# Optimization experiments

Measured on AMD Instinct MI355X. Metric: run time of the kernel, lower is better.

## Reference

```python
import jax, jax.numpy as jnp
import numpy as np

H = 768; B = 8; T = 1024; V = 50257
S = 256      # token_distribution_samples
K = 64       # token_topk
POOL = 1024  # max(S*4, K) token pool
TEMP = 0.1; LIM = 0.25; MW = 0.1


def _ln(x, g, b):
    m = x.mean(-1, keepdims=True)
    v = ((x - m) ** 2).mean(-1, keepdims=True)
    return (x - m) / jnp.sqrt(v + 1e-5) * g + b


def _head(x, g, b, w1, b1, w2, b2):
    # LayerNorm -> Linear -> GELU(exact) -> (Dropout=identity in eval) -> Linear
    h = _ln(x, g, b) @ w1 + b1
    h = jax.nn.gelu(h, approximate=False)
    return h @ w2 + b2


def _l2norm(x):
    return x / jnp.maximum(jnp.linalg.norm(x, axis=-1, keepdims=True), 1e-12)


def setup_inputs() -> dict:
    key = jax.random.key(0)
    ks = jax.random.split(key, 16)
    init = lambda k, shp: jax.random.normal(k, shp, jnp.float32) * 0.02
    f32 = jnp.float32
    return {
        "latent": jax.random.normal(ks[0], (B, T, H), f32),
        "token_embedding_matrix": jax.random.normal(ks[1], (V, H), f32),
        # scale head
        "scale_ln_g": jnp.ones((H,), f32), "scale_ln_b": jnp.zeros((H,), f32),
        "scale_w1": init(ks[2], (H, H)), "scale_b1": jnp.zeros((H,), f32),
        "scale_w2": init(ks[3], (H, H)), "scale_b2": jnp.zeros((H,), f32),
        # bias head
        "bias_ln_g": jnp.ones((H,), f32), "bias_ln_b": jnp.zeros((H,), f32),
        "bias_w1": init(ks[4], (H, H)), "bias_b1": jnp.zeros((H,), f32),
        "bias_w2": init(ks[5], (H, H)), "bias_b2": jnp.zeros((H,), f32),
        # contrastive head (projection_dim == H)
        "con_ln_g": jnp.ones((H,), f32), "con_ln_b": jnp.zeros((H,), f32),
        "con_w1": init(ks[6], (H, H)), "con_b1": jnp.zeros((H,), f32),
        "con_w2": init(ks[7], (H, H)), "con_b2": jnp.zeros((H,), f32),
        # deterministic augmentation noise (randn_like * 0.01)
        "noise_a": jax.random.normal(ks[8], (B * T, H), f32) * 0.01,
        "noise_b": jax.random.normal(ks[9], (B * T, H), f32) * 0.01,
        # deterministic row-sampling (torch.randperm analogues)
        "samp_idx": jax.random.permutation(ks[10], B * T)[:S].astype(jnp.int32),
        "tok_idx": jax.random.permutation(ks[11], V)[:POOL].astype(jnp.int32),
    }


def reference(latent, token_embedding_matrix,
              scale_ln_g, scale_ln_b, scale_w1, scale_b1, scale_w2, scale_b2,
              bias_ln_g, bias_ln_b, bias_w1, bias_b1, bias_w2, bias_b2,
              con_ln_g, con_ln_b, con_w1, con_b1, con_w2, con_b2,
              noise_a, noise_b, samp_idx, tok_idx):
    # compensate: u = s(z)*z + b(z)
    scale = 1.0 + LIM * jnp.tanh(_head(latent, scale_ln_g, scale_ln_b, scale_w1, scale_b1, scale_w2, scale_b2))
    bias = LIM * jnp.tanh(_head(latent, bias_ln_g, bias_ln_b, bias_w1, bias_b1, bias_w2, bias_b2))
    aligned = scale * latent + bias

    flat = aligned.reshape(-1, H)  # [N, H], N = B*T
    # contrastive loss
    va = _l2norm(_head(flat + noise_a, con_ln_g, con_ln_b, con_w1, con_b1, con_w2, con_b2))
    vb = _l2norm(_head(flat + noise_b, con_ln_g, con_ln_b, con_w1, con_b1, con_w2, con_b2))
    logits = va @ vb.T / TEMP  # [N, N]
    loss_ab = -jnp.mean(jnp.diagonal(jax.nn.log_softmax(logits, axis=-1)))
    loss_ba = -jnp.mean(jnp.diagonal(jax.nn.log_softmax(logits.T, axis=-1)))
    con_loss = 0.5 * (loss_ab + loss_ba)

    # token distribution loss
    af = flat[samp_idx]                     # [S, H]
    te = token_embedding_matrix[tok_idx]    # [POOL, H]
    tl = _l2norm(af) @ _l2norm(te).T / TEMP  # [S, POOL]
    top_vals, top_idx = jax.lax.top_k(tl, K)
    top_emb = te[top_idx]                   # [S, K, H] gather
    w = jax.nn.softmax(top_vals, axis=-1)[..., None]
    proto = (w * top_emb).sum(axis=1)       # [S, H]
    proto_loss = jnp.mean((af - proto) ** 2)
    moment_loss = jnp.mean((af.mean(0) - te.mean(0)) ** 2) \
        + jnp.mean((af.std(0) - te.std(0)) ** 2)
    token_dist_loss = proto_loss + MW * moment_loss

    comp_reg_loss = jnp.mean((scale - 1.0) ** 2) + jnp.mean(bias ** 2)
    return (aligned, con_loss, token_dist_loss, comp_reg_loss, scale, bias)
```

## Files before the change

### kernel.cpp

```cpp
#include <hip/hip_runtime.h>
#include <hip/hip_bf16.h>

typedef __hip_bfloat16 bf16;
typedef __attribute__((ext_vector_type(4))) float f32x4;
typedef __attribute__((ext_vector_type(8))) short bf16x8v;

static constexpr int   HD    = 768;
static constexpr int   NRr   = 8192;
static constexpr int   SSAMP = 256;
static constexpr int   KTOP  = 64;
static constexpr int   NPOOL = 1024;
static constexpr float TINV  = 10.0f;

__device__ __forceinline__ float bf2f(bf16 h){ return __bfloat162float(h); }
__device__ __forceinline__ bf16  f2bf(float f){ return __float2bfloat16(f); }

__device__ __forceinline__ float gelu_exact(float x){
  return 0.5f * x * (1.0f + erff(x * 0.70710678118654752f));
}

__device__ __forceinline__ float block_sum(float v, float* buf){
  const int lane = threadIdx.x & 63, w = threadIdx.x >> 6;
  const int nw = (int)blockDim.x >> 6;
  #pragma unroll
  for(int o = 32; o; o >>= 1) v += __shfl_down(v, o);
  __syncthreads();
  if(lane == 0) buf[w] = v;
  __syncthreads();
  float t = 0.f;
  for(int i = 0; i < nw; i++) t += buf[i];
  return t;
}

__device__ __forceinline__ void block_sum2(float& a, float& b, float* buf){
  const int lane = threadIdx.x & 63, w = threadIdx.x >> 6;
  #pragma unroll
  for(int o = 32; o; o >>= 1){ a += __shfl_down(a, o); b += __shfl_down(b, o); }
  __syncthreads();
  if(lane == 0){ buf[w] = a; buf[4 + w] = b; }
  __syncthreads();
  float ta = 0.f, tb = 0.f;
  #pragma unroll
  for(int i = 0; i < 4; i++){ ta += buf[i]; tb += buf[4 + i]; }
  a = ta; b = tb;
}

__device__ __forceinline__ void gload_lds16(const bf16* g, bf16* lds_uniform){
  __builtin_amdgcn_global_load_lds(
      (const __attribute__((address_space(1))) unsigned int*)(const void*)g,
      (__attribute__((address_space(3))) unsigned int*)(void*)lds_uniform,
      16, 0, 0);
}

struct TsA { const float* w[6]; const float* gg[6]; bf16* o[6]; };
__global__ __launch_bounds__(256)
void tscale6(TsA a){
  __shared__ float t[32][33];
  const int z = blockIdx.z;
  const float* Win = a.w[z];
  const float* g   = a.gg[z];
  bf16* Wt         = a.o[z];
  const int tx = threadIdx.x, ty = threadIdx.y;
  const int bx = blockIdx.x * 32, by = blockIdx.y * 32;
  #pragma unroll
  for(int j = 0; j < 4; j++)
    t[ty + j*8][tx] = Win[(size_t)(by + ty + j*8) * HD + bx + tx];
  __syncthreads();
  const float gv = g ? g[by + tx] : 1.0f;
  #pragma unroll
  for(int j = 0; j < 4; j++)
    Wt[(size_t)(bx + ty + j*8) * HD + by + tx] = f2bf(gv * t[tx][ty + j*8]);
}

struct FbA { const float* bln[3]; const float* w1[3]; const float* b1[3]; float* o[3]; };
__global__ __launch_bounds__(256)
void foldbias3(FbA a){
  __shared__ float red[4][64];
  const int h = blockIdx.y;
  const int lane = threadIdx.x & 63, w = threadIdx.x >> 6;
  const int n = blockIdx.x * 64 + lane;
  const float* bl = a.bln[h];
  const float* w1 = a.w1[h];
  float t = 0.f;
  for(int k = w * 192; k < w * 192 + 192; k++)
    t += bl[k] * w1[(size_t)k * HD + n];
  red[w][lane] = t;
  __syncthreads();
  if(w == 0)
    a.o[h][n] = a.b1[h][n] + red[0][lane] + red[1][lane] + red[2][lane] + red[3][lane];
}

__global__ __launch_bounds__(256)
void lnxh_kernel(const float* __restrict__ x, bf16* __restrict__ o){
  __shared__ float buf[4];
  const int row = blockIdx.x, tid = threadIdx.x;
  const size_t base = (size_t)row * HD;
  float v[3];
  #pragma unroll
  for(int j = 0; j < 3; j++) v[j] = x[base + tid + j*256];
  float s = v[0] + v[1] + v[2];
  s = block_sum(s, buf);
  const float m = s * (1.0f / HD);
  float q = 0.f;
  #pragma unroll
  for(int j = 0; j < 3; j++){ const float d = v[j] - m; q += d*d; }
  q = block_sum(q, buf);
  const float inv = rsqrtf(q * (1.0f / HD) + 1e-5f);
  #pragma unroll
  for(int j = 0; j < 3; j++)
    o[base + tid + j*256] = f2bf((v[j] - m) * inv);
}

__global__ __launch_bounds__(256)
void fuse_al_ln(const float* __restrict__ latent, const float* __restrict__ sc,
                const float* __restrict__ bi, const float* __restrict__ na,
                const float* __restrict__ nb, float* __restrict__ out_aligned,
                bf16* __restrict__ X){
  __shared__ float buf[8];
  const int row = blockIdx.x, tid = threadIdx.x;
  const size_t base = (size_t)row * HD;
  float ua[3], ub[3];
  #pragma unroll
  for(int j = 0; j < 3; j++){
    const int i = tid + j*256;
    const float a = sc[base + i] * latent[base + i] + bi[base + i];
    out_aligned[base + i] = a;
    ua[j] = a + na[base + i];
    ub[j] = a + nb[base + i];
  }
  float sa = ua[0] + ua[1] + ua[2];
  float sb = ub[0] + ub[1] + ub[2];
  block_sum2(sa, sb, buf);
  const float ma = sa * (1.0f / HD), mb = sb * (1.0f / HD);
  float qa = 0.f, qb = 0.f;
  #pragma unroll
  for(int j = 0; j < 3; j++){
    const float da = ua[j] - ma; qa += da*da;
    const float db = ub[j] - mb; qb += db*db;
  }
  block_sum2(qa, qb, buf);
  const float ia = rsqrtf(qa * (1.0f / HD) + 1e-5f);
  const float ib = rsqrtf(qb * (1.0f / HD) + 1e-5f);
  #pragma unroll
  for(int j = 0; j < 3; j++){
    const int i = tid + j*256;
    X[base + i] = f2bf((ua[j] - ma) * ia);
    X[(size_t)(row + NRr) * HD + i] = f2bf((ub[j] - mb) * ib);
  }
}

enum { EPI_GELU = 0, EPI_SB = 1, EPI_RAW = 3, EPI_LOGITS = 4, EPI_TL = 5 };

template<int EPI>
__global__ __launch_bounds__(256, 2)
void gemm_kernel(const bf16* __restrict__ A, const bf16* __restrict__ Bt,
                 const bf16* __restrict__ Bt2,
                 const int M, const int N, const int K,
                 const int lda, const int ldc,
                 const float* __restrict__ bias, const float* __restrict__ bias2,
                 bf16* __restrict__ outb, float* __restrict__ outf,
                 float* __restrict__ outf2,
                 float* __restrict__ aux, float* __restrict__ aux2){
  __shared__ __align__(16) bf16 As[128 * 64];
  __shared__ __align__(16) bf16 Bs[128 * 64];
  __shared__ float rbuf[512];

  const int tid  = threadIdx.x;
  const int wave = tid >> 6, lane = tid & 63;
  const int wm = wave >> 1, wn = wave & 1;
  const int r16 = lane & 15, kh = lane >> 4;
  const int bx = blockIdx.x, by = blockIdx.y;
  const int row0 = by * 128, col0 = bx * 128;

  float addv = 0.f;
  if constexpr(EPI == EPI_SB){
    if(blockIdx.z == 0){ addv = 1.0f; }
    else { A += 768; Bt = Bt2; bias = bias2; outf = outf2; }
  }

  f32x4 acc[4][4];
  #pragma unroll
  for(int i = 0; i < 4; i++)
    #pragma unroll
    for(int j = 0; j < 4; j++){ f32x4 z = {0.f,0.f,0.f,0.f}; acc[i][j] = z; }

  const bf16* gA[4]; const bf16* gB[4];
  bf16* lA[4]; bf16* lB[4];
  #pragma unroll
  for(int j = 0; j < 4; j++){
    const int c = tid + j*256;
    const int rr = c >> 3, p = c & 7;
    const int g = (p - (rr & 7)) & 7;
    gA[j] = A  + (size_t)(row0 + rr) * lda + g * 8;
    gB[j] = Bt + (size_t)(col0 + rr) * K   + g * 8;
    lA[j] = As + ((size_t)j*256 + wave*64) * 8;
    lB[j] = Bs + ((size_t)j*256 + wave*64) * 8;
  }
  const int sw = r16 & 7;

  for(int k0 = 0; k0 < K; k0 += 64){
    __syncthreads();
    #pragma unroll
    for(int j = 0; j < 4; j++){
      gload_lds16(gA[j] + k0, lA[j]);
      gload_lds16(gB[j] + k0, lB[j]);
    }
    __syncthreads();
    #pragma unroll
    for(int kk = 0; kk < 2; kk++){
      const int koff = ((kk*4 + kh + sw) & 7) * 8;
      bf16x8v av[4], bv[4];
      #pragma unroll
      for(int f = 0; f < 4; f++){
        av[f] = *(const bf16x8v*)(As + (wm*64 + f*16 + r16) * 64 + koff);
        bv[f] = *(const bf16x8v*)(Bs + (wn*64 + f*16 + r16) * 64 + koff);
      }
      #pragma unroll
      for(int i = 0; i < 4; i++)
        #pragma unroll
        for(int j = 0; j < 4; j++)
          acc[i][j] = __builtin_amdgcn_mfma_f32_16x16x32_bf16(av[i], bv[j], acc[i][j], 0, 0, 0);
    }
  }

  const int crow0 = row0 + wm * 64;
  const int ccol0 = col0 + wn * 64;

  if constexpr(EPI != EPI_LOGITS){
    float part = 0.f;
    #pragma unroll
    for(int i = 0; i < 4; i++){
      #pragma unroll
      for(int j = 0; j < 4; j++){
        const int col = ccol0 + j*16 + r16;
        const float bvv = bias ? bias[col] : 0.f;
        #pragma unroll
        for(int q = 0; q < 4; q++){
          const int row = crow0 + i*16 + kh*4 + q;
          const float v = acc[i][j][q] + bvv;
          const size_t off = (size_t)row * ldc + col;
          if constexpr(EPI == EPI_GELU){
            outb[off] = f2bf(gelu_exact(v));
          } else if constexpr(EPI == EPI_SB){
            const float t = 0.25f * tanhf(v);
            outf[off] = t + addv;
            part += t * t;
          } else if constexpr(EPI == EPI_TL){
            outf[off] = v * TINV;
          } else {
            outb[off] = f2bf(v);
          }
        }
      }
    }
    if constexpr(EPI == EPI_SB){
      const float tot2 = block_sum(part, rbuf);
      if(tid == 0)
        aux[(size_t)blockIdx.z * (gridDim.x * gridDim.y) + by * gridDim.x + bx] = tot2;
    }
  } else {
    float rs[16], cs[4];
    #pragma unroll
    for(int t = 0; t < 16; t++) rs[t] = 0.f;
    #pragma unroll
    for(int t = 0; t < 4; t++) cs[t] = 0.f;
    #pragma unroll
    for(int i = 0; i < 4; i++)
      #pragma unroll
      for(int j = 0; j < 4; j++)
        #pragma unroll
        for(int q = 0; q < 4; q++){
          const float ev = expf(acc[i][j][q] * TINV);
          rs[i*4 + q] += ev;
          cs[j]       += ev;
        }
    #pragma unroll
    for(int t = 0; t < 16; t++){
      float r = rs[t];
      r += __shfl_xor(r, 1); r += __shfl_xor(r, 2);
      r += __shfl_xor(r, 4); r += __shfl_xor(r, 8);
      rs[t] = r;
    }
    if(r16 == 0){
      #pragma unroll
      for(int i = 0; i < 4; i++)
        #pragma unroll
        for(int q = 0; q < 4; q++)
          rbuf[wn*128 + wm*64 + i*16 + kh*4 + q] = rs[i*4 + q];
    }
    #pragma unroll
    for(int j = 0; j < 4; j++){
      float c = cs[j];
      c += __shfl_xor(c, 16); c += __shfl_xor(c, 32);
      cs[j] = c;
    }
    if(kh == 0){
      #pragma unroll
      for(int j = 0; j < 4; j++)
        rbuf[256 + wm*128 + wn*64 + j*16 + r16] = cs[j];
    }
    __syncthreads();
    if(tid < 128){
      aux [(size_t)bx * M + row0 + tid] = rbuf[tid]       + rbuf[128 + tid];
      aux2[(size_t)by * M + col0 + tid] = rbuf[256 + tid] + rbuf[384 + tid];
    }
  }
}

__global__ __launch_bounds__(256)
void l2n_kernel(bf16* __restrict__ vio){
  __shared__ float buf[4];
  const int row = blockIdx.x, tid = threadIdx.x;
  const size_t base = (size_t)row * HD;
  float v[3];
  #pragma unroll
  for(int j = 0; j < 3; j++) v[j] = bf2f(vio[base + tid + j*256]);
  float q = v[0]*v[0] + v[1]*v[1] + v[2]*v[2];
  q = block_sum(q, buf);
  const float inv = 1.0f / fmaxf(sqrtf(q), 1e-12f);
  #pragma unroll
  for(int j = 0; j < 3; j++) vio[base + tid + j*256] = f2bf(v[j] * inv);
}

__global__ __launch_bounds__(256)
void diag_kernel(const bf16* __restrict__ va, const bf16* __restrict__ vb,
                 float* __restrict__ diag){
  const int lane = threadIdx.x & 63;
  const int row = blockIdx.x * 4 + (threadIdx.x >> 6);
  const size_t base = (size_t)row * HD;
  float d = 0.f;
  #pragma unroll
  for(int j = 0; j < 12; j++){
    const int i = lane + j*64;
    d += bf2f(va[base + i]) * bf2f(vb[base + i]);
  }
  #pragma unroll
  for(int o = 32; o; o >>= 1) d += __shfl_down(d, o);
  if(lane == 0) diag[row] = d * TINV;
}

__global__ __launch_bounds__(256)
void rcsum_kernel(const float* __restrict__ rp, const float* __restrict__ cp,
                  float* __restrict__ rs, float* __restrict__ cs, const int nb){
  const int i = blockIdx.x * 256 + threadIdx.x;
  float r = 0.f, c = 0.f;
  for(int b = 0; b < nb; b++){
    r += rp[(size_t)b * NRr + i];
    c += cp[(size_t)b * NRr + i];
  }
  rs[i] = r; cs[i] = c;
}

__global__ __launch_bounds__(256)
void af_kernel(const float* __restrict__ aligned, const int* __restrict__ samp,
               float* __restrict__ afraw, bf16* __restrict__ afn){
  __shared__ float buf[4];
  const int s = blockIdx.x, tid = threadIdx.x;
  const size_t src = (size_t)samp[s] * HD, dst = (size_t)s * HD;
  float v[3];
  #pragma unroll
  for(int j = 0; j < 3; j++){
    const int i = tid + j*256;
    v[j] = aligned[src + i];
    afraw[dst + i] = v[j];
  }
  float q = v[0]*v[0] + v[1]*v[1] + v[2]*v[2];
  q = block_sum(q, buf);
  const float inv = 1.0f / fmaxf(sqrtf(q), 1e-12f);
  #pragma unroll
  for(int j = 0; j < 3; j++) afn[dst + tid + j*256] = f2bf(v[j] * inv);
}

__global__ __launch_bounds__(256)
void te_kernel(const float* __restrict__ emb, const int* __restrict__ tok,
               float* __restrict__ teg, bf16* __restrict__ ten){
  __shared__ float buf[4];
  const int p = blockIdx.x, tid = threadIdx.x;
  const size_t src = (size_t)tok[p] * HD, dst = (size_t)p * HD;
  float v[3];
  #pragma unroll
  for(int j = 0; j < 3; j++){
    const int i = tid + j*256;
    v[j] = emb[src + i];
    teg[dst + i] = v[j];
  }
  float q = v[0]*v[0] + v[1]*v[1] + v[2]*v[2];
  q = block_sum(q, buf);
  const float inv = 1.0f / fmaxf(sqrtf(q), 1e-12f);
  #pragma unroll
  for(int j = 0; j < 3; j++) ten[dst + tid + j*256] = f2bf(v[j] * inv);
}

__global__ __launch_bounds__(256)
void topk_kernel(const float* __restrict__ tl, const float* __restrict__ teg,
                 const float* __restrict__ afraw, float* __restrict__ protopart){
  __shared__ float sv[NPOOL];
  __shared__ float topv[KTOP];
  __shared__ int   topi[KTOP];
  __shared__ float wts[KTOP];
  __shared__ float rv[4];
  __shared__ int   ri[4];
  __shared__ float buf[4];
  __shared__ float sinv;
  const int s = blockIdx.x, tid = threadIdx.x;
  const int lane = tid & 63, w = tid >> 6;
  #pragma unroll
  for(int j = 0; j < 4; j++) sv[tid + j*256] = tl[(size_t)s * NPOOL + tid + j*256];
  __syncthreads();
  for(int k = 0; k < KTOP; k++){
    float bvv = -1e30f; int bi = 0x7fffffff;
    #pragma unroll
    for(int j = 0; j < 4; j++){
      const int i = tid + j*256;
      const float x = sv[i];
      if(x > bvv || (x == bvv && i < bi)){ bvv = x; bi = i; }
    }
    #pragma unroll
    for(int o = 1; o < 64; o <<= 1){
      const float ov = __shfl_xor(bvv, o);
      const int   oi = __shfl_xor(bi, o);
      if(ov > bvv || (ov == bvv && oi < bi)){ bvv = ov; bi = oi; }
    }
    if(lane == 0){ rv[w] = bvv; ri[w] = bi; }
    __syncthreads();
    if(tid == 0){
      for(int w2 = 1; w2 < 4; w2++)
        if(rv[w2] > bvv || (rv[w2] == bvv && ri[w2] < bi)){ bvv = rv[w2]; bi = ri[w2]; }
      if(bi < 0 || bi >= NPOOL) bi = 0;
      topv[k] = bvv; topi[k] = bi; sv[bi] = -1e30f;
    }
    __syncthreads();
  }
  if(tid < KTOP) wts[tid] = expf(topv[tid] - topv[0]);
  __syncthreads();
  if(tid == 0){
    float t = 0.f;
    for(int k = 0; k < KTOP; k++) t += wts[k];
    sinv = 1.0f / t;
  }
  __syncthreads();
  float part = 0.f;
  #pragma unroll
  for(int j = 0; j < 3; j++){
    const int h = tid + j*256;
    float ph = 0.f;
    for(int k = 0; k < KTOP; k++) ph += wts[k] * teg[(size_t)topi[k] * HD + h];
    ph *= sinv;
    const float d = afraw[(size_t)s * HD + h] - ph;
    part += d * d;
  }
  part = block_sum(part, buf);
  if(tid == 0) protopart[s] = part;
}

__global__ __launch_bounds__(768)
void mom1_kernel(const float* __restrict__ afraw, const float* __restrict__ teg,
                 float* __restrict__ partial){
  const int b = blockIdx.x, h = threadIdx.x;
  float sa = 0.f, sa2 = 0.f, st = 0.f, st2 = 0.f;
  for(int r = b * 40; r < b * 40 + 40; r++){
    if(r < SSAMP){
      const float v = afraw[(size_t)r * HD + h];
      sa += v; sa2 += v * v;
    } else {
      const float v = teg[(size_t)(r - SSAMP) * HD + h];
      st += v; st2 += v * v;
    }
  }
  partial[(size_t)(b*4 + 0) * HD + h] = sa;
  partial[(size_t)(b*4 + 1) * HD + h] = sa2;
  partial[(size_t)(b*4 + 2) * HD + h] = st;
  partial[(size_t)(b*4 + 3) * HD + h] = st2;
}

__global__ __launch_bounds__(768)
void mom2_kernel(const float* __restrict__ partial, float* __restrict__ mom){
  __shared__ float buf[12];
  const int h = threadIdx.x;
  float sa = 0.f, sa2 = 0.f, st = 0.f, st2 = 0.f;
  for(int b = 0; b < 32; b++){
    sa  += partial[(size_t)(b*4 + 0) * HD + h];
    sa2 += partial[(size_t)(b*4 + 1) * HD + h];
    st  += partial[(size_t)(b*4 + 2) * HD + h];
    st2 += partial[(size_t)(b*4 + 3) * HD + h];
  }
  const float ma  = sa * (1.0f / SSAMP);
  const float sda = sqrtf(fmaxf(sa2 * (1.0f / SSAMP) - ma * ma, 0.f));
  const float mt  = st * (1.0f / NPOOL);
  const float sdt = sqrtf(fmaxf(st2 * (1.0f / NPOOL) - mt * mt, 0.f));
  const float dmu = ma - mt, dsd = sda - sdt;
  const float t1 = block_sum(dmu * dmu, buf);
  const float t2 = block_sum(dsd * dsd, buf);
  if(h == 0){ mom[0] = t1; mom[1] = t2; }
}

__global__ __launch_bounds__(1024)
void final_kernel(const float* __restrict__ rs, const float* __restrict__ cs,
                  const float* __restrict__ diag,
                  const float* __restrict__ aux, const int naux,
                  const float* __restrict__ protopart, const float* __restrict__ mom,
                  float* __restrict__ outsc){
  __shared__ float buf[16];
  const int tid = threadIdx.x;
  float s1 = 0.f, s2 = 0.f;
  for(int r = tid; r < NRr; r += 1024){
    const float dg = diag[r];
    s1 += logf(rs[r]) - dg;
    s2 += logf(cs[r]) - dg;
  }
  float c1 = 0.f;
  for(int j = tid; j < naux; j += 1024) c1 += aux[j];
  float pp = 0.f;
  for(int j = tid; j < SSAMP; j += 1024) pp += protopart[j];
  s1 = block_sum(s1, buf);
  s2 = block_sum(s2, buf);
  c1 = block_sum(c1, buf);
  pp = block_sum(pp, buf);
  if(tid == 0){
    const float con  = 0.5f * (s1 + s2) / (float)NRr;
    const float creg = c1 / 6291456.0f;
    const float tdl  = pp / (float)(SSAMP * HD) + 0.1f * ((mom[0] + mom[1]) / (float)HD);
    outsc[0] = con;
    outsc[1] = tdl;
    outsc[2] = creg;
  }
}

extern "C" void kernel_launch(void* const* d_in, const int* in_sizes, int n_in,
                              void* d_out, int out_size, void* d_ws, size_t ws_size,
                              hipStream_t stream){
  (void)in_sizes; (void)n_in; (void)out_size; (void)ws_size;
  const float* latent = (const float*)d_in[0];
  const float* tokemb = (const float*)d_in[1];
  const float* s_g  = (const float*)d_in[2];  const float* s_bln = (const float*)d_in[3];
  const float* s_w1 = (const float*)d_in[4];  const float* s_b1  = (const float*)d_in[5];
  const float* s_w2 = (const float*)d_in[6];  const float* s_b2  = (const float*)d_in[7];
  const float* b_g  = (const float*)d_in[8];  const float* b_bln = (const float*)d_in[9];
  const float* b_w1 = (const float*)d_in[10]; const float* b_b1  = (const float*)d_in[11];
  const float* b_w2 = (const float*)d_in[12]; const float* b_b2  = (const float*)d_in[13];
  const float* c_g  = (const float*)d_in[14]; const float* c_bln = (const float*)d_in[15];
  const float* c_w1 = (const float*)d_in[16]; const float* c_b1  = (const float*)d_in[17];
  const float* c_w2 = (const float*)d_in[18]; const float* c_b2  = (const float*)d_in[19];
  const float* noise_a = (const float*)d_in[20];
  const float* noise_b = (const float*)d_in[21];
  const int*  samp = (const int*)d_in[22];
  const int*  tok  = (const int*)d_in[23];

  float* out = (float*)d_out;
  float* out_aligned = out;
  float* out_scalars = out + (size_t)NRr * HD;
  float* out_scale   = out + (size_t)NRr * HD + 3;
  float* out_bias    = out_scale + (size_t)NRr * HD;

  char* wp = (char*)d_ws;
  auto alloc = [&](size_t bytes) -> char* {
    char* p = wp; wp += (bytes + 255) & ~(size_t)255; return p;
  };
  bf16* wt_comb1 = (bf16*)alloc((size_t)2*HD*HD*2);
  bf16* wt_c1    = (bf16*)alloc((size_t)HD*HD*2);
  bf16* wt_s2    = (bf16*)alloc((size_t)HD*HD*2);
  bf16* wt_b2    = (bf16*)alloc((size_t)HD*HD*2);
  bf16* wt_c2    = (bf16*)alloc((size_t)HD*HD*2);
  float* bcomb1  = (float*)alloc(2*HD*4);
  float* bc1     = (float*)alloc(HD*4);
  bf16* A1 = (bf16*)alloc((size_t)2*NRr*HD*2);
  bf16* A2 = (bf16*)alloc((size_t)2*NRr*HD*2);
  float* rowpart = (float*)alloc((size_t)64*NRr*4);
  float* colpart = (float*)alloc((size_t)64*NRr*4);
  float* rowsum  = (float*)alloc((size_t)NRr*4);
  float* colsum  = (float*)alloc((size_t)NRr*4);
  float* diag    = (float*)alloc((size_t)NRr*4);
  float* aux     = (float*)alloc(768*4);
  float* afraw   = (float*)alloc((size_t)SSAMP*HD*4);
  float* teg     = (float*)alloc((size_t)NPOOL*HD*4);
  float* tlb     = (float*)alloc((size_t)SSAMP*NPOOL*4);
  float* protopart = (float*)alloc(SSAMP*4);
  float* mom     = (float*)alloc(2*4);
  float* mompart = rowpart;
  bf16*  ten     = (bf16*)colpart;
  bf16*  afn     = (bf16*)(colpart + ((size_t)NPOOL*HD*2)/4);

  TsA ts;
  ts.w[0]=s_w1; ts.gg[0]=s_g;     ts.o[0]=wt_comb1;
  ts.w[1]=b_w1; ts.gg[1]=b_g;     ts.o[1]=wt_comb1 + (size_t)HD*HD;
  ts.w[2]=c_w1; ts.gg[2]=c_g;     ts.o[2]=wt_c1;
  ts.w[3]=s_w2; ts.gg[3]=nullptr; ts.o[3]=wt_s2;
  ts.w[4]=b_w2; ts.gg[4]=nullptr; ts.o[4]=wt_b2;
  ts.w[5]=c_w2; ts.gg[5]=nullptr; ts.o[5]=wt_c2;
  tscale6<<<dim3(24,24,6), dim3(32,8), 0, stream>>>(ts);
  FbA fb;
  fb.bln[0]=s_bln; fb.w1[0]=s_w1; fb.b1[0]=s_b1; fb.o[0]=bcomb1;
  fb.bln[1]=b_bln; fb.w1[1]=b_w1; fb.b1[1]=b_b1; fb.o[1]=bcomb1 + HD;
  fb.bln[2]=c_bln; fb.w1[2]=c_w1; fb.b1[2]=c_b1; fb.o[2]=bc1;
  foldbias3<<<dim3(12,3), 256, 0, stream>>>(fb);

  lnxh_kernel<<<NRr, 256, 0, stream>>>(latent, A2);
  gemm_kernel<EPI_GELU><<<dim3(12,64), 256, 0, stream>>>(
      A2, wt_comb1, nullptr, NRr, 2*HD, HD, HD, 2*HD, bcomb1, nullptr,
      A1, nullptr, nullptr, nullptr, nullptr);
  gemm_kernel<EPI_SB><<<dim3(6,64,2), 256, 0, stream>>>(
      A1, wt_s2, wt_b2, NRr, HD, HD, 2*HD, HD, s_b2, b_b2,
      nullptr, out_scale, out_bias, aux, nullptr);

  fuse_al_ln<<<NRr, 256, 0, stream>>>(latent, out_scale, out_bias,
                                      noise_a, noise_b, out_aligned, A1);

  gemm_kernel<EPI_GELU><<<dim3(6,128), 256, 0, stream>>>(
      A1, wt_c1, nullptr, 2*NRr, HD, HD, HD, HD, bc1, nullptr,
      A2, nullptr, nullptr, nullptr, nullptr);
  gemm_kernel<EPI_RAW><<<dim3(6,128), 256, 0, stream>>>(
      A2, wt_c2, nullptr, 2*NRr, HD, HD, HD, HD, c_b2, nullptr,
      A1, nullptr, nullptr, nullptr, nullptr);
  l2n_kernel<<<2*NRr, 256, 0, stream>>>(A1);
  bf16* va = A1;
  bf16* vb = A1 + (size_t)NRr * HD;

  gemm_kernel<EPI_LOGITS><<<dim3(64,64), 256, 0, stream>>>(
      va, vb, nullptr, NRr, NRr, HD, HD, 0, nullptr, nullptr,
      nullptr, nullptr, nullptr, rowpart, colpart);
  rcsum_kernel<<<NRr / 256, 256, 0, stream>>>(rowpart, colpart, rowsum, colsum, 64);
  diag_kernel<<<NRr / 4, 256, 0, stream>>>(va, vb, diag);

  af_kernel<<<SSAMP, 256, 0, stream>>>(out_aligned, samp, afraw, afn);
  te_kernel<<<NPOOL, 256, 0, stream>>>(tokemb, tok, teg, ten);
  gemm_kernel<EPI_TL><<<dim3(8,2), 256, 0, stream>>>(
      afn, ten, nullptr, SSAMP, NPOOL, HD, HD, NPOOL, nullptr, nullptr,
      nullptr, tlb, nullptr, nullptr, nullptr);
  topk_kernel<<<SSAMP, 256, 0, stream>>>(tlb, teg, afraw, protopart);
  mom1_kernel<<<32, 768, 0, stream>>>(afraw, teg, mompart);
  mom2_kernel<<<1, 768, 0, stream>>>(mompart, mom);

  final_kernel<<<1, 1024, 0, stream>>>(rowsum, colsum, diag, aux, 768,
                                       protopart, mom, out_scalars);
}
```

Before: 518.1 us.

## Replace logits GEMM with 256x256-tile 8-wave pipelined kernel using direct-to-LDS loads

The 8192x8192 contrastive logits GEMM with fused exp row and column sums moves to a dedicated kernel. It uses 256x256 tiles, 512 threads, double-buffered direct global-to-LDS loads, interleaved stage, read and MFMA phases with explicit waitcnt and barriers, and raised priority around the MFMA bursts. The larger tile halves the operand reloads per output, and the hand pipelining overlaps loads with matrix math. In exchange it needs heavy register use (one block per CU), large LDS, and a fragile manual schedule, and row and column partials are now reduced over 32 tiles instead of 64.

```diff
diff --git a/kernel.cpp b/kernel.cpp
--- a/kernel.cpp
+++ b/kernel.cpp
@@ -149,7 +149,7 @@
   }
 }
 
-enum { EPI_GELU = 0, EPI_SB = 1, EPI_RAW = 3, EPI_LOGITS = 4, EPI_TL = 5 };
+enum { EPI_GELU = 0, EPI_SB = 1, EPI_RAW = 3, EPI_TL = 5 };
 
 template<int EPI>
 __global__ __launch_bounds__(256, 2)
@@ -160,7 +160,7 @@
                  const float* __restrict__ bias, const float* __restrict__ bias2,
                  bf16* __restrict__ outb, float* __restrict__ outf,
                  float* __restrict__ outf2,
-                 float* __restrict__ aux, float* __restrict__ aux2){
+                 float* __restrict__ aux){
   __shared__ __align__(16) bf16 As[128 * 64];
   __shared__ __align__(16) bf16 Bs[128 * 64];
   __shared__ float rbuf[512];
@@ -226,86 +226,194 @@
   const int crow0 = row0 + wm * 64;
   const int ccol0 = col0 + wn * 64;
 
-  if constexpr(EPI != EPI_LOGITS){
-    float part = 0.f;
-    #pragma unroll
-    for(int i = 0; i < 4; i++){
+  float part = 0.f;
+  #pragma unroll
+  for(int i = 0; i < 4; i++){
+    #pragma unroll
+    for(int j = 0; j < 4; j++){
+      const int col = ccol0 + j*16 + r16;
+      const float bvv = bias ? bias[col] : 0.f;
       #pragma unroll
-      for(int j = 0; j < 4; j++){
-        const int col = ccol0 + j*16 + r16;
-        const float bvv = bias ? bias[col] : 0.f;
-        #pragma unroll
-        for(int q = 0; q < 4; q++){
-          const int row = crow0 + i*16 + kh*4 + q;
-          const float v = acc[i][j][q] + bvv;
-          const size_t off = (size_t)row * ldc + col;
-          if constexpr(EPI == EPI_GELU){
-            outb[off] = f2bf(gelu_exact(v));
-          } else if constexpr(EPI == EPI_SB){
-            const float t = 0.25f * tanhf(v);
-            outf[off] = t + addv;
-            part += t * t;
-          } else if constexpr(EPI == EPI_TL){
-            outf[off] = v * TINV;
-          } else {
-            outb[off] = f2bf(v);
-          }
+      for(int q = 0; q < 4; q++){
+        const int row = crow0 + i*16 + kh*4 + q;
+        const float v = acc[i][j][q] + bvv;
+        const size_t off = (size_t)row * ldc + col;
+        if constexpr(EPI == EPI_GELU){
+          outb[off] = f2bf(gelu_exact(v));
+        } else if constexpr(EPI == EPI_SB){
+          const float t = 0.25f * tanhf(v);
+          outf[off] = t + addv;
+          part += t * t;
+        } else if constexpr(EPI == EPI_TL){
+          outf[off] = v * TINV;
+        } else {
+          outb[off] = f2bf(v);
         }
       }
     }
-    if constexpr(EPI == EPI_SB){
-      const float tot2 = block_sum(part, rbuf);
-      if(tid == 0)
-        aux[(size_t)blockIdx.z * (gridDim.x * gridDim.y) + by * gridDim.x + bx] = tot2;
+  }
+  if constexpr(EPI == EPI_SB){
+    const float tot2 = block_sum(part, rbuf);
+    if(tid == 0)
+      aux[(size_t)blockIdx.z * (gridDim.x * gridDim.y) + by * gridDim.x + bx] = tot2;
+  }
+}
+
+#define SYNC1 __builtin_amdgcn_s_barrier();                                  \
+  asm volatile("s_waitcnt lgkmcnt(0)" ::: "memory");                         \
+  __builtin_amdgcn_sched_barrier(0);
+#define SYNC2 __builtin_amdgcn_s_barrier();                                  \
+  __builtin_amdgcn_sched_barrier(0);
+#define VMC(n) asm volatile("s_waitcnt vmcnt(" #n ")" ::: "memory");
+#define STAGE(b, mat, h, t1)                                                 \
+  { const bf16* s_ = (mat) ? srcB : srcA;                                    \
+    bf16* d_ = &lds[b][mat][0];                                              \
+    gload_lds16(s_ + (size_t)((h)*64) * HD + (t1)*64,                        \
+                d_ + ((h)*64)*64 + ldsu);                                    \
+    gload_lds16(s_ + (size_t)(128 + (h)*64) * HD + (t1)*64,                  \
+                d_ + (128 + (h)*64)*64 + ldsu); }
+#define RDA(b, mh)                                                           \
+  { const bf16* p_ = &lds[b][0][0];                                          \
+    _Pragma("unroll")                                                        \
+    for(int m = 0; m < 4; m++){                                              \
+      av[m][0] = *(const bf16x8v*)(p_ + (wm*128 + (mh)*64 + m*16 + r16)*64 + poff0); \
+      av[m][1] = *(const bf16x8v*)(p_ + (wm*128 + (mh)*64 + m*16 + r16)*64 + poff1); \
+    } }
+#define RDB(b, nh, bvv)                                                      \
+  { const bf16* p_ = &lds[b][1][0];                                          \
+    _Pragma("unroll")                                                        \
+    for(int n = 0; n < 2; n++){                                              \
+      bvv[n][0] = *(const bf16x8v*)(p_ + (wn*64 + (nh)*32 + n*16 + r16)*64 + poff0); \
+      bvv[n][1] = *(const bf16x8v*)(p_ + (wn*64 + (nh)*32 + n*16 + r16)*64 + poff1); \
+    } }
+#define MFMA16(mh, nh, bvv)                                                  \
+  __builtin_amdgcn_s_setprio(1);                                             \
+  _Pragma("unroll")                                                          \
+  for(int m = 0; m < 4; m++)                                                 \
+    _Pragma("unroll")                                                        \
+    for(int n = 0; n < 2; n++){                                              \
+      acc[(mh)*4+m][(nh)*2+n] = __builtin_amdgcn_mfma_f32_16x16x32_bf16(     \
+          av[m][0], bvv[n][0], acc[(mh)*4+m][(nh)*2+n], 0, 0, 0);            \
+      acc[(mh)*4+m][(nh)*2+n] = __builtin_amdgcn_mfma_f32_16x16x32_bf16(     \
+          av[m][1], bvv[n][1], acc[(mh)*4+m][(nh)*2+n], 0, 0, 0);            \
+    }                                                                        \
+  __builtin_amdgcn_s_setprio(0);
+
+__global__ __launch_bounds__(512, 1)
+void logits8p_kernel(const bf16* __restrict__ A, const bf16* __restrict__ Bt,
+                     float* __restrict__ rowp, float* __restrict__ colp){
+  __shared__ __align__(16) bf16 lds[2][2][256*64];
+  __shared__ float red[1536];
+
+  const int tid  = threadIdx.x;
+  const int wave = tid >> 6, lane = tid & 63;
+  const int wm = wave >> 2, wn = wave & 3;
+  const int r16 = lane & 15, kh = lane >> 4;
+  const int row0 = blockIdx.y * 256, col0 = blockIdx.x * 256;
+  const int nt = HD / 64;
+
+  const int grow = tid >> 3;
+  const int glg8 = (((tid & 7) - ((tid >> 3) & 7)) & 7) * 8;
+  const bf16* srcA = A  + (size_t)(row0 + grow) * HD + glg8;
+  const bf16* srcB = Bt + (size_t)(col0 + grow) * HD + glg8;
+  const int ldsu = wave * 512;
+
+  const int sw = r16 & 7;
+  const int poff0 = ((kh + sw) & 7) * 8;
+  const int poff1 = ((4 + kh + sw) & 7) * 8;
+
+  f32x4 acc[8][4];
+  #pragma unroll
+  for(int i = 0; i < 8; i++)
+    #pragma unroll
+    for(int j = 0; j < 4; j++){ f32x4 z = {0.f,0.f,0.f,0.f}; acc[i][j] = z; }
+
+  STAGE(0, 0, 0, 0);
+  STAGE(0, 1, 0, 0);
+  STAGE(0, 1, 1, 0);
+  STAGE(0, 0, 1, 0);
+  VMC(4)
+  __builtin_amdgcn_s_barrier();
+  __builtin_amdgcn_sched_barrier(0);
+
+  bf16x8v av[4][2], bv0[2][2], bv1[2][2];
+
+  for(int t = 0; t < nt; t++){
+    const int b = t & 1, nb2 = b ^ 1;
+    const bool st = (t + 1 < nt);
+    if(st) STAGE(nb2, 0, 0, t+1)
+    RDA(b, 0)
+    RDB(b, 0, bv0)
+    SYNC1
+    MFMA16(0, 0, bv0)
+    if(st){ VMC(4) } else { VMC(2) }
+    SYNC2
+    if(st) STAGE(nb2, 1, 0, t+1)
+    RDB(b, 1, bv1)
+    SYNC1
+    MFMA16(0, 1, bv1)
+    if(st){ VMC(4) } else { VMC(0) }
+    SYNC2
+    if(st) STAGE(nb2, 1, 1, t+1)
+    RDA(b, 1)
+    SYNC1
+    MFMA16(1, 1, bv1)
+    SYNC2
+    if(st) STAGE(nb2, 0, 1, t+1)
+    SYNC1
+    MFMA16(1, 0, bv0)
+    if(st){ VMC(4) }
+    SYNC2
+  }
+
+  float rsumv[8][4];
+  float csumv[4];
+  #pragma unroll
+  for(int i = 0; i < 8; i++)
+    #pragma unroll
+    for(int q = 0; q < 4; q++) rsumv[i][q] = 0.f;
+  #pragma unroll
+  for(int j = 0; j < 4; j++) csumv[j] = 0.f;
+  #pragma unroll
+  for(int i = 0; i < 8; i++)
+    #pragma unroll
+    for(int j = 0; j < 4; j++)
+      #pragma unroll
+      for(int q = 0; q < 4; q++){
+        const float ev = expf(acc[i][j][q] * TINV);
+        rsumv[i][q] += ev;
+        csumv[j]    += ev;
+      }
+  #pragma unroll
+  for(int i = 0; i < 8; i++)
+    #pragma unroll
+    for(int q = 0; q < 4; q++){
+      float v = rsumv[i][q];
+      v += __shfl_xor(v, 1); v += __shfl_xor(v, 2);
+      v += __shfl_xor(v, 4); v += __shfl_xor(v, 8);
+      if(r16 == 0) red[wn*256 + wm*128 + i*16 + kh*4 + q] = v;
     }
-  } else {
-    float rs[16], cs[4];
-    #pragma unroll
-    for(int t = 0; t < 16; t++) rs[t] = 0.f;
-    #pragma unroll
-    for(int t = 0; t < 4; t++) cs[t] = 0.f;
-    #pragma unroll
-    for(int i = 0; i < 4; i++)
-      #pragma unroll
-      for(int j = 0; j < 4; j++)
-        #pragma unroll
-        for(int q = 0; q < 4; q++){
-          const float ev = expf(acc[i][j][q] * TINV);
-          rs[i*4 + q] += ev;
-          cs[j]       += ev;
-        }
-    #pragma unroll
-    for(int t = 0; t < 16; t++){
-      float r = rs[t];
-      r += __shfl_xor(r, 1); r += __shfl_xor(r, 2);
-      r += __shfl_xor(r, 4); r += __shfl_xor(r, 8);
-      rs[t] = r;
-    }
-    if(r16 == 0){
-      #pragma unroll
-      for(int i = 0; i < 4; i++)
-        #pragma unroll
-        for(int q = 0; q < 4; q++)
-          rbuf[wn*128 + wm*64 + i*16 + kh*4 + q] = rs[i*4 + q];
-    }
-    #pragma unroll
-    for(int j = 0; j < 4; j++){
-      float c = cs[j];
-      c += __shfl_xor(c, 16); c += __shfl_xor(c, 32);
-      cs[j] = c;
-    }
-    if(kh == 0){
-      #pragma unroll
-      for(int j = 0; j < 4; j++)
-        rbuf[256 + wm*128 + wn*64 + j*16 + r16] = cs[j];
-    }
-    __syncthreads();
-    if(tid < 128){
-      aux [(size_t)bx * M + row0 + tid] = rbuf[tid]       + rbuf[128 + tid];
-      aux2[(size_t)by * M + col0 + tid] = rbuf[256 + tid] + rbuf[384 + tid];
-    }
-  }
-}
+  #pragma unroll
+  for(int j = 0; j < 4; j++){
+    float c = csumv[j];
+    c += __shfl_xor(c, 16); c += __shfl_xor(c, 32);
+    if(kh == 0) red[1024 + wm*256 + wn*64 + j*16 + r16] = c;
+  }
+  __syncthreads();
+  if(tid < 256){
+    rowp[(size_t)blockIdx.x * NRr + row0 + tid] =
+        red[tid] + red[256 + tid] + red[512 + tid] + red[768 + tid];
+    colp[(size_t)blockIdx.y * NRr + col0 + tid] =
+        red[1024 + tid] + red[1280 + tid];
+  }
+}
+#undef SYNC1
+#undef SYNC2
+#undef VMC
+#undef STAGE
+#undef RDA
+#undef RDB
+#undef MFMA16
 
 __global__ __launch_bounds__(256)
 void l2n_kernel(bf16* __restrict__ vio){
@@ -597,35 +705,33 @@
   lnxh_kernel<<<NRr, 256, 0, stream>>>(latent, A2);
   gemm_kernel<EPI_GELU><<<dim3(12,64), 256, 0, stream>>>(
       A2, wt_comb1, nullptr, NRr, 2*HD, HD, HD, 2*HD, bcomb1, nullptr,
-      A1, nullptr, nullptr, nullptr, nullptr);
+      A1, nullptr, nullptr, nullptr);
   gemm_kernel<EPI_SB><<<dim3(6,64,2), 256, 0, stream>>>(
       A1, wt_s2, wt_b2, NRr, HD, HD, 2*HD, HD, s_b2, b_b2,
-      nullptr, out_scale, out_bias, aux, nullptr);
+      nullptr, out_scale, out_bias, aux);
 
   fuse_al_ln<<<NRr, 256, 0, stream>>>(latent, out_scale, out_bias,
                                       noise_a, noise_b, out_aligned, A1);
 
   gemm_kernel<EPI_GELU><<<dim3(6,128), 256, 0, stream>>>(
       A1, wt_c1, nullptr, 2*NRr, HD, HD, HD, HD, bc1, nullptr,
-      A2, nullptr, nullptr, nullptr, nullptr);
+      A2, nullptr, nullptr, nullptr);
   gemm_kernel<EPI_RAW><<<dim3(6,128), 256, 0, stream>>>(
       A2, wt_c2, nullptr, 2*NRr, HD, HD, HD, HD, c_b2, nullptr,
-      A1, nullptr, nullptr, nullptr, nullptr);
+      A1, nullptr, nullptr, nullptr);
   l2n_kernel<<<2*NRr, 256, 0, stream>>>(A1);
   bf16* va = A1;
   bf16* vb = A1 + (size_t)NRr * HD;
 
-  gemm_kernel<EPI_LOGITS><<<dim3(64,64), 256, 0, stream>>>(
-      va, vb, nullptr, NRr, NRr, HD, HD, 0, nullptr, nullptr,
-      nullptr, nullptr, nullptr, rowpart, colpart);
-  rcsum_kernel<<<NRr / 256, 256, 0, stream>>>(rowpart, colpart, rowsum, colsum, 64);
+  logits8p_kernel<<<dim3(32,32), 512, 0, stream>>>(va, vb, rowpart, colpart);
+  rcsum_kernel<<<NRr / 256, 256, 0, stream>>>(rowpart, colpart, rowsum, colsum, 32);
   diag_kernel<<<NRr / 4, 256, 0, stream>>>(va, vb, diag);
 
   af_kernel<<<SSAMP, 256, 0, stream>>>(out_aligned, samp, afraw, afn);
   te_kernel<<<NPOOL, 256, 0, stream>>>(tokemb, tok, teg, ten);
   gemm_kernel<EPI_TL><<<dim3(8,2), 256, 0, stream>>>(
       afn, ten, nullptr, SSAMP, NPOOL, HD, HD, NPOOL, nullptr, nullptr,
-      nullptr, tlb, nullptr, nullptr, nullptr);
+      nullptr, tlb, nullptr, nullptr);
   topk_kernel<<<SSAMP, 256, 0, stream>>>(tlb, teg, afraw, protopart);
   mom1_kernel<<<32, 768, 0, stream>>>(afraw, teg, mompart);
   mom2_kernel<<<1, 768, 0, stream>>>(mompart, mom);
```

Measured after the change: 540.5 us. +4.3%, slower.
